# Optimization experiments

Measured on AMD Instinct MI355X. Metric: run time of the kernel, lower is better.

The kernel has to match this reference:

```python
import jax, jax.numpy as jnp
import numpy as np

N_ATOMS = 100000
N_EDGES = 625000
N_MOL = 1000
EMB_ATOM = 256
EMB_EDGE = 128


def setup_inputs() -> dict:
    key = jax.random.key(0)
    ks = jax.random.split(key, 8)
    h_energy = jax.random.normal(ks[0], (N_ATOMS, EMB_ATOM), dtype=jnp.float32)
    h_forces = jax.random.normal(ks[1], (N_EDGES, EMB_EDGE), dtype=jnp.float32)
    V_st = jax.random.normal(ks[2], (N_EDGES, 3), dtype=jnp.float32)
    idx_t = jax.random.randint(ks[3], (N_EDGES,), 0, N_ATOMS, dtype=jnp.int64)
    batch_idx = jnp.sort(jax.random.randint(ks[4], (N_ATOMS,), 0, N_MOL, dtype=jnp.int64))
    W_energy = jax.random.normal(ks[5], (EMB_ATOM, 1), dtype=jnp.float32) / np.sqrt(EMB_ATOM)
    W_forces = jax.random.normal(ks[6], (EMB_EDGE, 1), dtype=jnp.float32) / np.sqrt(EMB_EDGE)
    b_forces = jnp.zeros((1,), dtype=jnp.float32)
    return {
        "h_energy": h_energy,
        "h_forces": h_forces,
        "V_st": V_st,
        "idx_t": idx_t,
        "batch_idx": batch_idx,
        "W_energy": W_energy,
        "W_forces": W_forces,
        "b_forces": b_forces,
    }


def reference(h_energy, h_forces, V_st, idx_t, batch_idx, W_energy, W_forces, b_forces):
    # Energy head: per-atom linear (bias=False), scatter-sum over molecules.
    e_atom = h_energy @ W_energy                      # [N, 1]
    y = jax.ops.segment_sum(e_atom, batch_idx, num_segments=N_MOL)  # [B, 1]
    y = y[:, 0]                                       # rearrange 'b 1 -> b'
    # Forces head: per-edge linear, scale by unit edge vector V_st,
    # scatter-sum into target atoms idx_t.
    f_edge = (h_forces @ W_forces + b_forces) * V_st  # [E, 3] via broadcast of [E,1]
    force = jax.ops.segment_sum(f_edge, idx_t, num_segments=N_ATOMS)  # [N, 3]
    return y, force
```

## Files before the change

kernel.cpp:

```cpp
#include <hip/hip_runtime.h>

#define N_ATOMS 100000
#define N_EDGES 625000
#define N_MOL   1000
#define EMB_ATOM 256
#define EMB_EDGE 128

typedef float f32x4 __attribute__((ext_vector_type(4)));

__device__ __forceinline__ float dot4(f32x4 a, f32x4 b) {
    return a.x * b.x + a.y * b.y + a.z * b.z + a.w * b.w;
}

#define REP      8
#define YREP_STR 1024
#define FREP_OFF 8192
#define FREP_STR 300000
#define WS_FLOATS (FREP_OFF + REP * FREP_STR)

__global__ __launch_bounds__(256) void zero_kernel(f32x4* __restrict__ p, int n4)
{
    const int i = blockIdx.x * blockDim.x + threadIdx.x;
    if (i < n4) p[i] = (f32x4)(0.f, 0.f, 0.f, 0.f);
}

__global__ __launch_bounds__(256) void merge_kernel(
    const float* __restrict__ ws, float* __restrict__ out)
{
    const int i = blockIdx.x * blockDim.x + threadIdx.x;
    if (i >= 250 + 75000) return;
    const f32x4* w4 = reinterpret_cast<const f32x4*>(ws);
    f32x4*       o4 = reinterpret_cast<f32x4*>(out);
    if (i < 250) {
        f32x4 s = (f32x4)(0.f, 0.f, 0.f, 0.f);
        #pragma unroll
        for (int k = 0; k < REP; ++k) s += w4[i + k * (YREP_STR/4)];
        o4[i] = s;
    } else {
        const int j = i - 250;
        const f32x4* f4 = w4 + FREP_OFF/4;
        f32x4 s = (f32x4)(0.f, 0.f, 0.f, 0.f);
        #pragma unroll
        for (int k = 0; k < REP; ++k) s += f4[j + k * (FREP_STR/4)];
        o4[i] = s;
    }
}

#define FTILES  ((N_EDGES + 15) / 16)
#define FPBLOCKS 1960
#define ETILES  (N_ATOMS / 8)
#define EPBLOCKS 600

__global__ __launch_bounds__(256) void fused_kernel(
    const float* __restrict__ h_energy,
    const float* __restrict__ h_forces,
    const float* __restrict__ V_st,
    const int*   __restrict__ idx_t,
    const int*   __restrict__ batch_idx,
    const float* __restrict__ W_energy,
    const float* __restrict__ W_forces,
    const float* __restrict__ b_forces,
    float*       __restrict__ ws)
{
    const int lane = threadIdx.x & 63;

    if (blockIdx.x < FPBLOCKS) {
        const int wslot = blockIdx.x * 4 + (threadIdx.x >> 6);
        const int slot  = lane >> 3;
        const int sub   = lane & 7;

        const f32x4* wf   = reinterpret_cast<const f32x4*>(W_forces);
        const f32x4* base = reinterpret_cast<const f32x4*>(h_forces);
        float* frep = ws + FREP_OFF + (wslot & (REP-1)) * FREP_STR;

        f32x4 b0 = wf[sub + 0];
        f32x4 b1 = wf[sub + 8];
        f32x4 b2 = wf[sub + 16];
        f32x4 b3 = wf[sub + 24];
        const float bias = b_forces[0];

        for (int tile = wslot; tile < FTILES; tile += FPBLOCKS * 4) {
            #pragma unroll
            for (int g = 0; g < 2; ++g) {
                const int e = tile * 16 + g * 8 + slot;
                float s = 0.f;
                if (e < N_EDGES) {
                    const f32x4* row = base + (size_t)e * 32;
                    f32x4 a0 = row[sub + 0];
                    f32x4 a1 = row[sub + 8];
                    f32x4 a2 = row[sub + 16];
                    f32x4 a3 = row[sub + 24];
                    s = dot4(a0, b0) + dot4(a1, b1) + dot4(a2, b2) + dot4(a3, b3);
                }
                s += __shfl_xor(s, 1, 64);
                s += __shfl_xor(s, 2, 64);
                s += __shfl_xor(s, 4, 64);
                if (e < N_EDGES && sub < 3) {
                    const int   t = idx_t[e];
                    const float v = V_st[(size_t)e * 3 + sub];
                    atomicAdd(&frep[(size_t)t * 3 + sub], (s + bias) * v);
                }
            }
        }
    } else if (blockIdx.x < FPBLOCKS + EPBLOCKS) {
        const int wslot = (blockIdx.x - FPBLOCKS) * 4 + (threadIdx.x >> 6);
        const int slot  = lane >> 4;
        const int sub   = lane & 15;

        const f32x4* we   = reinterpret_cast<const f32x4*>(W_energy);
        const f32x4* base = reinterpret_cast<const f32x4*>(h_energy);
        float* yrep = ws + (wslot & (REP-1)) * YREP_STR;

        f32x4 b0 = we[sub + 0];
        f32x4 b1 = we[sub + 16];
        f32x4 b2 = we[sub + 32];
        f32x4 b3 = we[sub + 48];

        for (int tile = wslot; tile < ETILES; tile += EPBLOCKS * 4) {
            #pragma unroll
            for (int g = 0; g < 2; ++g) {
                const int a = tile * 8 + g * 4 + slot;
                const f32x4* row = base + (size_t)a * 64;
                f32x4 a0 = row[sub + 0];
                f32x4 a1 = row[sub + 16];
                f32x4 a2 = row[sub + 32];
                f32x4 a3 = row[sub + 48];
                float s = dot4(a0, b0) + dot4(a1, b1) + dot4(a2, b2) + dot4(a3, b3);

                s += __shfl_xor(s, 1, 64);
                s += __shfl_xor(s, 2, 64);
                s += __shfl_xor(s, 4, 64);
                s += __shfl_xor(s, 8, 64);

                if (sub == 0) atomicAdd(&yrep[batch_idx[a]], s);
            }
        }
    }
}

extern "C" void kernel_launch(void* const* d_in, const int* in_sizes, int n_in,
                              void* d_out, int out_size, void* d_ws, size_t ws_size,
                              hipStream_t stream) {
    const float* h_energy  = (const float*)d_in[0];
    const float* h_forces  = (const float*)d_in[1];
    const float* V_st      = (const float*)d_in[2];
    const int*   idx_t     = (const int*)d_in[3];
    const int*   batch_idx = (const int*)d_in[4];
    const float* W_energy  = (const float*)d_in[5];
    const float* W_forces  = (const float*)d_in[6];
    const float* b_forces  = (const float*)d_in[7];

    float* ws  = (float*)d_ws;
    float* out = (float*)d_out;

    const int zn4 = WS_FLOATS / 4;
    zero_kernel<<<(zn4 + 255) / 256, 256, 0, stream>>>((f32x4*)d_ws, zn4);

    fused_kernel<<<FPBLOCKS + EPBLOCKS, 256, 0, stream>>>(
        h_energy, h_forces, V_st, idx_t, batch_idx,
        W_energy, W_forces, b_forces, ws);

    merge_kernel<<<(75250 + 255) / 256, 256, 0, stream>>>(ws, out);
}
```

Baseline: 106.4 us.

## Stage edge rows via global_load_lds and unify work units across all waves

```diff
diff --git a/kernel.cpp b/kernel.cpp
--- a/kernel.cpp
+++ b/kernel.cpp
@@ -1,4 +1,5 @@
 #include <hip/hip_runtime.h>
+#include <stdint.h>
 
 #define N_ATOMS 100000
 #define N_EDGES 625000
@@ -7,6 +8,8 @@
 #define EMB_EDGE 128
 
 typedef float f32x4 __attribute__((ext_vector_type(4)));
+typedef __attribute__((address_space(1))) const uint32_t gu32;
+typedef __attribute__((address_space(3))) uint32_t su32;
 
 __device__ __forceinline__ float dot4(f32x4 a, f32x4 b) {
     return a.x * b.x + a.y * b.y + a.z * b.z + a.w * b.w;
@@ -47,9 +50,10 @@
 }
 
 #define FTILES  ((N_EDGES + 15) / 16)
-#define FPBLOCKS 1960
 #define ETILES  (N_ATOMS / 8)
-#define EPBLOCKS 600
+#define TOTAL_UNITS (FTILES + ETILES)
+#define NBLOCKS 1280
+#define NSLOTS  (NBLOCKS * 4)
 
 __global__ __launch_bounds__(256) void fused_kernel(
     const float* __restrict__ h_energy,
@@ -62,77 +66,86 @@
     const float* __restrict__ b_forces,
     float*       __restrict__ ws)
 {
-    const int lane = threadIdx.x & 63;
+    __shared__ __align__(16) char smem[4][8192];
 
-    if (blockIdx.x < FPBLOCKS) {
-        const int wslot = blockIdx.x * 4 + (threadIdx.x >> 6);
-        const int slot  = lane >> 3;
-        const int sub   = lane & 7;
+    const int lane  = threadIdx.x & 63;
+    const int widx  = threadIdx.x >> 6;
+    const int wslot = blockIdx.x * 4 + widx;
+    char* lbase = smem[widx];
 
-        const f32x4* wf   = reinterpret_cast<const f32x4*>(W_forces);
-        const f32x4* base = reinterpret_cast<const f32x4*>(h_forces);
-        float* frep = ws + FREP_OFF + (wslot & (REP-1)) * FREP_STR;
+    const int p    = lane & 31;
+    const int half = lane >> 5;
+    const f32x4* wf = reinterpret_cast<const f32x4*>(W_forces);
+    const f32x4  wb = wf[p];
+    const float bias = b_forces[0];
 
-        f32x4 b0 = wf[sub + 0];
-        f32x4 b1 = wf[sub + 8];
-        f32x4 b2 = wf[sub + 16];
-        f32x4 b3 = wf[sub + 24];
-        const float bias = b_forces[0];
+    const int esub  = lane & 15;
+    const int eslot = lane >> 4;
+    const f32x4* we = reinterpret_cast<const f32x4*>(W_energy);
+    const f32x4 eb0 = we[esub +  0];
+    const f32x4 eb1 = we[esub + 16];
+    const f32x4 eb2 = we[esub + 32];
+    const f32x4 eb3 = we[esub + 48];
 
-        for (int tile = wslot; tile < FTILES; tile += FPBLOCKS * 4) {
+    float* frep = ws + FREP_OFF + (wslot & (REP-1)) * FREP_STR;
+    float* yrep = ws + (wslot & (REP-1)) * YREP_STR;
+
+    const char*  fbase = reinterpret_cast<const char*>(h_forces);
+    const f32x4* ebase4 = reinterpret_cast<const f32x4*>(h_energy);
+
+    for (int u = wslot; u < TOTAL_UNITS; u += NSLOTS) {
+        if (u < FTILES) {
+            const int e0 = u * 16;
+            const char* gsrc = fbase + (size_t)e0 * 512 + (size_t)lane * 16;
+
+            #pragma unroll
+            for (int j = 0; j < 8; ++j) {
+                if (e0 + 2*j < N_EDGES) {
+                    __builtin_amdgcn_global_load_lds(
+                        (gu32*)(const void*)(gsrc + j * 1024),
+                        (su32*)(void*)(lbase + j * 1024),
+                        16, 0, 0);
+                }
+            }
+            asm volatile("s_waitcnt vmcnt(0)" ::: "memory");
+            __builtin_amdgcn_sched_barrier(0);
+
+            #pragma unroll
+            for (int j = 0; j < 8; ++j) {
+                const int e = e0 + 2*j + half;
+                if (e0 + 2*j < N_EDGES) {
+                    f32x4 r = *reinterpret_cast<const f32x4*>(lbase + j * 1024 + lane * 16);
+                    float s = dot4(r, wb);
+                    s += __shfl_xor(s, 1, 64);
+                    s += __shfl_xor(s, 2, 64);
+                    s += __shfl_xor(s, 4, 64);
+                    s += __shfl_xor(s, 8, 64);
+                    s += __shfl_xor(s, 16, 64);
+                    if (p < 3 && e < N_EDGES) {
+                        const int   t = idx_t[e];
+                        const float v = V_st[(size_t)e * 3 + p];
+                        atomicAdd(&frep[(size_t)t * 3 + p], (s + bias) * v);
+                    }
+                }
+            }
+        } else {
+            const int tile = u - FTILES;
             #pragma unroll
             for (int g = 0; g < 2; ++g) {
-                const int e = tile * 16 + g * 8 + slot;
-                float s = 0.f;
-                if (e < N_EDGES) {
-                    const f32x4* row = base + (size_t)e * 32;
-                    f32x4 a0 = row[sub + 0];
-                    f32x4 a1 = row[sub + 8];
-                    f32x4 a2 = row[sub + 16];
-                    f32x4 a3 = row[sub + 24];
-                    s = dot4(a0, b0) + dot4(a1, b1) + dot4(a2, b2) + dot4(a3, b3);
-                }
-                s += __shfl_xor(s, 1, 64);
-                s += __shfl_xor(s, 2, 64);
-                s += __shfl_xor(s, 4, 64);
-                if (e < N_EDGES && sub < 3) {
-                    const int   t = idx_t[e];
-                    const float v = V_st[(size_t)e * 3 + sub];
-                    atomicAdd(&frep[(size_t)t * 3 + sub], (s + bias) * v);
-                }
-            }
-        }
-    } else if (blockIdx.x < FPBLOCKS + EPBLOCKS) {
-        const int wslot = (blockIdx.x - FPBLOCKS) * 4 + (threadIdx.x >> 6);
-        const int slot  = lane >> 4;
-        const int sub   = lane & 15;
-
-        const f32x4* we   = reinterpret_cast<const f32x4*>(W_energy);
-        const f32x4* base = reinterpret_cast<const f32x4*>(h_energy);
-        float* yrep = ws + (wslot & (REP-1)) * YREP_STR;
-
-        f32x4 b0 = we[sub + 0];
-        f32x4 b1 = we[sub + 16];
-        f32x4 b2 = we[sub + 32];
-        f32x4 b3 = we[sub + 48];
-
-        for (int tile = wslot; tile < ETILES; tile += EPBLOCKS * 4) {
-            #pragma unroll
-            for (int g = 0; g < 2; ++g) {
-                const int a = tile * 8 + g * 4 + slot;
-                const f32x4* row = base + (size_t)a * 64;
-                f32x4 a0 = row[sub + 0];
-                f32x4 a1 = row[sub + 16];
-                f32x4 a2 = row[sub + 32];
-                f32x4 a3 = row[sub + 48];
-                float s = dot4(a0, b0) + dot4(a1, b1) + dot4(a2, b2) + dot4(a3, b3);
+                const int a = tile * 8 + g * 4 + eslot;
+                const f32x4* row = ebase4 + (size_t)a * 64;
+                f32x4 a0 = __builtin_nontemporal_load(row + esub + 0);
+                f32x4 a1 = __builtin_nontemporal_load(row + esub + 16);
+                f32x4 a2 = __builtin_nontemporal_load(row + esub + 32);
+                f32x4 a3 = __builtin_nontemporal_load(row + esub + 48);
+                float s = dot4(a0, eb0) + dot4(a1, eb1) + dot4(a2, eb2) + dot4(a3, eb3);
 
                 s += __shfl_xor(s, 1, 64);
                 s += __shfl_xor(s, 2, 64);
                 s += __shfl_xor(s, 4, 64);
                 s += __shfl_xor(s, 8, 64);
 
-                if (sub == 0) atomicAdd(&yrep[batch_idx[a]], s);
+                if (esub == 0) atomicAdd(&yrep[batch_idx[a]], s);
             }
         }
     }
@@ -156,7 +169,7 @@
     const int zn4 = WS_FLOATS / 4;
     zero_kernel<<<(zn4 + 255) / 256, 256, 0, stream>>>((f32x4*)d_ws, zn4);
 
-    fused_kernel<<<FPBLOCKS + EPBLOCKS, 256, 0, stream>>>(
+    fused_kernel<<<NBLOCKS, 256, 0, stream>>>(
         h_energy, h_forces, V_st, idx_t, batch_idx,
         W_energy, W_forces, b_forces, ws);
 
```

New measurement: 145.6 us. 36.9% more time.
